# Optimization experiments

Measured on AMD Instinct MI355X. Metric: run time of the kernel, lower is better.

The kernel has to match this reference:

```python
import jax, jax.numpy as jnp
import numpy as np

B, N, DIM = 4, 2048, 256
HEADS, CODEBOOK, HD = 4, 8192, 64  # HD = DIM // HEADS


def setup_inputs() -> dict:
    key = jax.random.key(0)
    k1, k2 = jax.random.split(key)
    x = jax.random.normal(k1, (B, N, DIM), dtype=jnp.float32)
    embed = jax.random.normal(k2, (HEADS, CODEBOOK, HD), dtype=jnp.float32)
    return {"x": x, "embed": embed}


def reference(x, embed):
    b, n, dim = x.shape
    h, c, d = embed.shape
    # 'b n (h d) -> h b n d' then pack to 'h (b n) d'
    flat = x.reshape(b, n, h, d).transpose(2, 0, 1, 3).reshape(h, b * n, d)
    x2 = jnp.sum(flat * flat, axis=-1)              # [h, bn]
    y2 = jnp.sum(embed * embed, axis=-1)            # [h, c]
    xy = jnp.einsum('hmd,hcd->hmc', flat, embed)    # [h, bn, c]
    sq = x2[:, :, None] + y2[:, None, :] - 2.0 * xy
    dist = -jnp.sqrt(jnp.maximum(sq, 0.0))          # clamp for fp safety
    embed_ind = jnp.argmax(dist, axis=-1)           # [h, bn]
    # gather codes per head
    quantize = jnp.take_along_axis(embed, embed_ind[:, :, None], axis=1)  # [h, bn, d]
    # 'h (b n) d -> b n (h d)'
    quantize = quantize.reshape(h, b, n, d).transpose(1, 2, 0, 3).reshape(b, n, h * d)
    # 'h (b n) -> b n h'
    embed_ind = embed_ind.reshape(h, b, n).transpose(1, 2, 0)
    return quantize, embed_ind
```

## Files before the change

### kernel.cpp

```cpp
#include <hip/hip_runtime.h>
#include <hip/hip_bf16.h>


#define HEADS    4
#define CODEBOOK 8192
#define HD       64
#define BQ       8192
#define QOFF     (4 * 2048 * 256)
#define NPART    8
#define CPART    (CODEBOOK / NPART)
#define SCODES   64
#define NSTAGE   (CPART / SCODES)
#define RSCALE   4096.0f
#define RINV     (1.0f / 4096.0f)

typedef _Float16 f16x8 __attribute__((ext_vector_type(8)));
typedef float    f32x4 __attribute__((ext_vector_type(4)));

__device__ float g_pval[NPART][HEADS * BQ];
__device__ int   g_pidx[NPART][HEADS * BQ];

__device__ inline void split2(float f, _Float16& h0, _Float16& h1) {
    h0 = (_Float16)f;
    float r = f - (float)h0;
    h1 = (_Float16)(r * RSCALE);
}

__global__ __launch_bounds__(256, 2) void dist_kernel(const float* __restrict__ x,
                                                      const float* __restrict__ embed) {
    __shared__ __align__(16) _Float16 tile[2][2][SCODES * 64];
    __shared__ float y2s[CPART];

    const int bid  = blockIdx.x;
    const int part = bid & 7;
    const int qg   = (bid >> 3) & 31;
    const int h    = bid >> 8;
    const int t    = threadIdx.x;
    const int wave = t >> 6;
    const int lane = t & 63;
    const int col  = lane & 15;
    const int quad = lane >> 4;

    const int qbase = qg * 256 + wave * 64;
    const int cbase = part * CPART;

    f16x8 a[4][2][2];
#pragma unroll
    for (int rt = 0; rt < 4; rt++) {
#pragma unroll
        for (int kh = 0; kh < 2; kh++) {
            const float* p = x + ((size_t)(qbase + rt * 16 + col) * 256 + h * 64 + kh * 32 + quad * 8);
#pragma unroll
            for (int j = 0; j < 8; j++) {
                _Float16 h0, h1;
                split2(p[j], h0, h1);
                a[rt][0][kh][j] = h0;
                a[rt][1][kh][j] = h1;
            }
        }
    }

    const float* esrc = embed + ((size_t)h * CODEBOOK + cbase) * HD + (size_t)t * 8;
    const int row  = t >> 3;
    const int gsw  = (t & 7) ^ (row & 7);
    const int ldA  = row * 64 + gsw * 8;
    const int ldB  = (row + 32) * 64 + gsw * 8;

    float bv[4][4]; int bc[4][4];
#pragma unroll
    for (int rt = 0; rt < 4; rt++)
#pragma unroll
        for (int r = 0; r < 4; r++) { bv[rt][r] = -3.4e38f; bc[rt][r] = 0; }

    float4 pfA0, pfA1, pfB0, pfB1;

    auto stage_write = [&](int buf, int stage) {
        float fA[8] = {pfA0.x, pfA0.y, pfA0.z, pfA0.w, pfA1.x, pfA1.y, pfA1.z, pfA1.w};
        float fB[8] = {pfB0.x, pfB0.y, pfB0.z, pfB0.w, pfB1.x, pfB1.y, pfB1.z, pfB1.w};
        f16x8 vA0, vA1, vB0, vB1;
        float ssA = 0.f, ssB = 0.f;
#pragma unroll
        for (int j = 0; j < 8; j++) {
            _Float16 h0, h1;
            split2(fA[j], h0, h1);
            vA0[j] = h0; vA1[j] = h1;
            ssA = fmaf(fA[j], fA[j], ssA);
            split2(fB[j], h0, h1);
            vB0[j] = h0; vB1[j] = h1;
            ssB = fmaf(fB[j], fB[j], ssB);
        }
        *reinterpret_cast<f16x8*>(&tile[buf][0][ldA]) = vA0;
        *reinterpret_cast<f16x8*>(&tile[buf][1][ldA]) = vA1;
        *reinterpret_cast<f16x8*>(&tile[buf][0][ldB]) = vB0;
        *reinterpret_cast<f16x8*>(&tile[buf][1][ldB]) = vB1;
#pragma unroll
        for (int off = 4; off >= 1; off >>= 1) {
            ssA += __shfl_xor(ssA, off, 8);
            ssB += __shfl_xor(ssB, off, 8);
        }
        if ((t & 7) == 0) {
            y2s[stage * SCODES + row]      = -0.5f * ssA;
            y2s[stage * SCODES + row + 32] = -0.5f * ssB;
        }
    };
    auto stage_load = [&](int stage) {
        const float* ps = esrc + (size_t)stage * (SCODES * HD);
        pfA0 = *reinterpret_cast<const float4*>(ps);
        pfA1 = *reinterpret_cast<const float4*>(ps + 4);
        pfB0 = *reinterpret_cast<const float4*>(ps + 32 * HD);
        pfB1 = *reinterpret_cast<const float4*>(ps + 32 * HD + 4);
    };

    stage_load(0);
    stage_write(0, 0);
    stage_load(1);
    __syncthreads();

    const int swbase = col & 7;
    const f32x4 z4 = {0.f, 0.f, 0.f, 0.f};

    for (int s = 0; s < NSTAGE; s++) {
        if (s + 1 < NSTAGE) stage_write((s + 1) & 1, s + 1);
        if (s + 2 < NSTAGE) stage_load(s + 2);

#pragma unroll
        for (int inner = 0; inner < 4; inner++) {
            const int rbase = (inner * 16 + col) * 64;
            f16x8 b[2][2];
#pragma unroll
            for (int lvl = 0; lvl < 2; lvl++)
#pragma unroll
                for (int kh = 0; kh < 2; kh++)
                    b[lvl][kh] = *reinterpret_cast<const f16x8*>(
                        &tile[s & 1][lvl][rbase + ((((kh << 2) | quad) ^ swbase) << 3)]);

            const int   c   = s * SCODES + inner * 16 + col;
            const float ycn = y2s[c];
#pragma unroll
            for (int rt = 0; rt < 4; rt++) {
                __builtin_amdgcn_s_setprio(1);
                f32x4 aA = __builtin_amdgcn_mfma_f32_16x16x32_f16(a[rt][0][0], b[0][0], z4, 0, 0, 0);
                f32x4 aB = __builtin_amdgcn_mfma_f32_16x16x32_f16(a[rt][0][0], b[1][0], z4, 0, 0, 0);
                aB = __builtin_amdgcn_mfma_f32_16x16x32_f16(a[rt][1][0], b[0][0], aB, 0, 0, 0);
                aA = __builtin_amdgcn_mfma_f32_16x16x32_f16(a[rt][0][1], b[0][1], aA, 0, 0, 0);
                aB = __builtin_amdgcn_mfma_f32_16x16x32_f16(a[rt][0][1], b[1][1], aB, 0, 0, 0);
                aB = __builtin_amdgcn_mfma_f32_16x16x32_f16(a[rt][1][1], b[0][1], aB, 0, 0, 0);
                __builtin_amdgcn_s_setprio(0);
#pragma unroll
                for (int r = 0; r < 4; r++) {
                    float sv = fmaf(aB[r], RINV, aA[r] + ycn);
                    if (sv > bv[rt][r]) { bv[rt][r] = sv; bc[rt][r] = c; }
                }
            }
        }
        __syncthreads();
    }

#pragma unroll
    for (int rt = 0; rt < 4; rt++) {
#pragma unroll
        for (int r = 0; r < 4; r++) {
            float v = bv[rt][r]; int c = bc[rt][r];
#pragma unroll
            for (int off = 8; off >= 1; off >>= 1) {
                float ov = __shfl_xor(v, off, 16); int oc = __shfl_xor(c, off, 16);
                if (ov > v || (ov == v && oc < c)) { v = ov; c = oc; }
            }
            if (col == 0) {
                int q = h * BQ + qbase + rt * 16 + quad * 4 + r;
                g_pval[part][q] = v; g_pidx[part][q] = cbase + c;
            }
        }
    }
}

__global__ __launch_bounds__(256) void merge_kernel(const float* __restrict__ embed,
                                                    float* __restrict__ out) {
    __shared__ int iw[32][4];
    const int t     = threadIdx.x;
    const int mbase = blockIdx.x * 32;

    if (t < 128) {
        const int ml = t >> 2;
        const int h  = t & 3;
        const int q  = h * BQ + mbase + ml;
        float bv = g_pval[0][q]; int bc = g_pidx[0][q];
#pragma unroll
        for (int p = 1; p < NPART; p++) {
            float v = g_pval[p][q]; int c = g_pidx[p][q];
            if (v > bv || (v == bv && c < bc)) { bv = v; bc = c; }
        }
        out[QOFF + (size_t)mbase * 4 + t] = (float)bc;
        iw[ml][h] = bc & (CODEBOOK - 1);
    }
    __syncthreads();

    const int wave = t >> 6;
    const int lane = t & 63;
    const int h    = lane >> 4;
    const int off  = (lane & 15) * 4;
#pragma unroll
    for (int i = 0; i < 8; i++) {
        const int r   = wave * 8 + i;
        const int m   = mbase + r;
        const int idx = iw[r][h];
        const float4 v = *reinterpret_cast<const float4*>(
            embed + ((size_t)h * CODEBOOK + idx) * HD + off);
        *reinterpret_cast<float4*>(out + (size_t)m * 256 + lane * 4) = v;
    }
}

extern "C" void kernel_launch(void* const* d_in, const int* in_sizes, int n_in,
                              void* d_out, int out_size, void* d_ws, size_t ws_size,
                              hipStream_t stream) {
    const float* x     = (const float*)d_in[0];
    const float* embed = (const float*)d_in[1];
    float*       out   = (float*)d_out;

    dist_kernel <<<1024, 256, 0, stream>>>(x, embed);
    merge_kernel<<<256,  256, 0, stream>>>(embed, out);
}
```

Baseline: 178.8 us.

## Fuse partition merge and gather into distance kernel via last-block atomic counter

Removes the separate merge kernel. Each dist block bumps a per-(head, query-group) atomic counter after writing its partial argmax, and the last of the eight partition blocks merges the partials and gathers the codebook rows into the output. This saves a kernel launch and the gap between kernels. In exchange it adds threadfence/atomic synchronisation and tail work on the finishing block, and the output writes are now strided per head.

```diff
diff --git a/kernel.cpp b/kernel.cpp
--- a/kernel.cpp
+++ b/kernel.cpp
@@ -19,6 +19,7 @@
 
 __device__ float g_pval[NPART][HEADS * BQ];
 __device__ int   g_pidx[NPART][HEADS * BQ];
+__device__ int   g_cnt[HEADS * 32];
 
 __device__ inline void split2(float f, _Float16& h0, _Float16& h1) {
     h0 = (_Float16)f;
@@ -27,9 +28,11 @@
 }
 
 __global__ __launch_bounds__(256, 2) void dist_kernel(const float* __restrict__ x,
-                                                      const float* __restrict__ embed) {
+                                                      const float* __restrict__ embed,
+                                                      float* __restrict__ out) {
     __shared__ __align__(16) _Float16 tile[2][2][SCODES * 64];
     __shared__ float y2s[CPART];
+    __shared__ int s_old;
 
     const int bid  = blockIdx.x;
     const int part = bid & 7;
@@ -172,41 +175,41 @@
             }
         }
     }
-}
-
-__global__ __launch_bounds__(256) void merge_kernel(const float* __restrict__ embed,
-                                                    float* __restrict__ out) {
-    __shared__ int iw[32][4];
-    const int t     = threadIdx.x;
-    const int mbase = blockIdx.x * 32;
-
-    if (t < 128) {
-        const int ml = t >> 2;
-        const int h  = t & 3;
-        const int q  = h * BQ + mbase + ml;
-        float bv = g_pval[0][q]; int bc = g_pidx[0][q];
+
+    const int grp = (h << 5) | qg;
+    __syncthreads();
+    __threadfence();
+    if (t == 0) s_old = atomicAdd(&g_cnt[grp], 1);
+    __syncthreads();
+    if (s_old != NPART - 1) return;
+
+    if (t == 0) atomicExch(&g_cnt[grp], 0);
+    __threadfence();
+
+    int* sidx = reinterpret_cast<int*>(y2s);
+    const int m0 = qg * 256;
+    {
+        const int q = h * BQ + m0 + t;
+        float mv = g_pval[0][q]; int mc = g_pidx[0][q];
 #pragma unroll
         for (int p = 1; p < NPART; p++) {
             float v = g_pval[p][q]; int c = g_pidx[p][q];
-            if (v > bv || (v == bv && c < bc)) { bv = v; bc = c; }
-        }
-        out[QOFF + (size_t)mbase * 4 + t] = (float)bc;
-        iw[ml][h] = bc & (CODEBOOK - 1);
-    }
-    __syncthreads();
-
-    const int wave = t >> 6;
-    const int lane = t & 63;
-    const int h    = lane >> 4;
-    const int off  = (lane & 15) * 4;
-#pragma unroll
-    for (int i = 0; i < 8; i++) {
-        const int r   = wave * 8 + i;
-        const int m   = mbase + r;
-        const int idx = iw[r][h];
+            if (v > mv || (v == mv && c < mc)) { mv = v; mc = c; }
+        }
+        out[QOFF + (size_t)(m0 + t) * 4 + h] = (float)mc;
+        sidx[t] = mc & (CODEBOOK - 1);
+    }
+    __syncthreads();
+
+    const int rr = lane >> 4;
+    const int fo = (lane & 15) * 4;
+#pragma unroll
+    for (int i = 0; i < 16; i++) {
+        const int r   = wave * 64 + i * 4 + rr;
+        const int idx = sidx[r];
         const float4 v = *reinterpret_cast<const float4*>(
-            embed + ((size_t)h * CODEBOOK + idx) * HD + off);
-        *reinterpret_cast<float4*>(out + (size_t)m * 256 + lane * 4) = v;
+            embed + ((size_t)h * CODEBOOK + idx) * HD + fo);
+        *reinterpret_cast<float4*>(out + (size_t)(m0 + r) * 256 + h * 64 + fo) = v;
     }
 }
 
@@ -217,6 +220,5 @@
     const float* embed = (const float*)d_in[1];
     float*       out   = (float*)d_out;
 
-    dist_kernel <<<1024, 256, 0, stream>>>(x, embed);
-    merge_kernel<<<256,  256, 0, stream>>>(embed, out);
+    dist_kernel<<<1024, 256, 0, stream>>>(x, embed, out);
 }
```

After: 320.2 us. 1.79x slower.
